# Kernel tuning notes

Hardware: AMD Instinct MI355X
Metric: run time of the kernel (lower is better)

## Reference

```python
import jax, jax.numpy as jnp
import numpy as np

EPS = 1e-8  # torch CosineSimilarity eps

M, N, D, H, NODE_NUM = 8, 100000, 256, 256, 200000

def setup_inputs() -> dict:
    key = jax.random.key(0)
    k1, k2, k3, k4, k5 = jax.random.split(key, 5)
    nodes = jax.random.randint(k1, (N,), 0, NODE_NUM)
    homo_embeddings = jax.random.normal(k2, (M, N, D), dtype=jnp.float32)
    W = jax.random.normal(k3, (H, D), dtype=jnp.float32) * (1.0 / np.sqrt(D))
    b = jax.random.normal(k4, (H,), dtype=jnp.float32) * 0.01
    out_embedding = jax.random.uniform(k5, (NODE_NUM, H), dtype=jnp.float32)  # nn.init.uniform_
    return {"nodes": nodes, "homo_embeddings": homo_embeddings, "W": W, "b": b,
            "out_embedding": out_embedding}

def reference(nodes, homo_embeddings, W, b, out_embedding):
    # homo_embeddings: [M, N, D] stacked homo_embedding_list
    # hidden = tanh(Linear(homo_emb))  -> [M, N, H]
    hidden = jnp.tanh(jnp.einsum('mnd,hd->mnh', homo_embeddings, W) + b)
    tgt = out_embedding[nodes]  # [N, H]
    # cosine similarity along feature dim, per meta-path -> [M, N]
    num = jnp.einsum('mnh,nh->mn', hidden, tgt)
    hn = jnp.maximum(jnp.linalg.norm(hidden, axis=-1), EPS)        # [M, N]
    tn = jnp.maximum(jnp.linalg.norm(tgt, axis=-1), EPS)           # [N]
    attention = jax.nn.softmax((num / (hn * tn[None, :])).T, axis=1)  # [N, M]
    # weighted sum over meta-paths -> [N, D]
    final = jnp.einsum('nm,mnd->nd', attention, homo_embeddings)
    return final
```

## Files before the change

kernel.cpp:

```cpp
#include <hip/hip_runtime.h>
#include <hip/hip_bf16.h>

#define EPSF 1e-8f
constexpr int M_ = 8, N_ = 100000, D_ = 256, H_ = 256;

typedef short  short8  __attribute__((ext_vector_type(8)));
typedef short  short4_ __attribute__((ext_vector_type(4)));
typedef float  float4_ __attribute__((ext_vector_type(4)));

__device__ __forceinline__ short bf16_rn(float x) {
  union { float f; unsigned u; } v; v.f = x;
  unsigned r = v.u + 0x7FFFu + ((v.u >> 16) & 1u);
  return (short)(r >> 16);
}

#define XB_S 264
#define XF_S 257
#define TG_S 260

__global__ __launch_bounds__(256, 2) void fused_hete(
    const int* __restrict__ nodes, const float* __restrict__ homo,
    const float* __restrict__ W, const float* __restrict__ bias,
    const float* __restrict__ oute, float* __restrict__ out)
{
  __shared__ __align__(16) short xb[16 * XB_S];
  __shared__ __align__(16) float xf[16 * XF_S];
  __shared__ __align__(16) float tg[2 * TG_S];
  __shared__ float rnum[4][16];
  __shared__ float rhn[4][16];
  __shared__ float cos_s[16];
  __shared__ float att_s[2][8];
  __shared__ float tn_s[2];

  const int t    = threadIdx.x;
  const int wave = t >> 6, lane = t & 63;
  const int quad = lane >> 4, l16 = lane & 15;

  short8 wf[4][8];
  float  bcol[4];
  #pragma unroll
  for (int tt = 0; tt < 4; ++tt) {
    const int col = wave * 64 + tt * 16 + l16;
    bcol[tt] = bias[col];
    #pragma unroll
    for (int k0 = 0; k0 < 8; ++k0) {
      const float* wp = W + (size_t)col * D_ + k0 * 32 + quad * 8;
      short8 f;
      #pragma unroll
      for (int j = 0; j < 8; ++j) f[j] = bf16_rn(wp[j]);
      wf[tt][k0] = f;
    }
  }

  for (int pair = blockIdx.x; pair < N_ / 2; pair += gridDim.x) {
    const int n0 = pair * 2;

    {
      const int r = t >> 4, c = t & 15;
      const int m = r & 7, ln = r >> 3;
      const float* src = homo + ((size_t)m * N_ + (n0 + ln)) * D_;
      #pragma unroll
      for (int i = 0; i < 4; ++i) {
        const int d = i * 64 + c * 4;
        const float4 v = *(const float4*)(src + d);
        float* xfr = &xf[r * XF_S + d];
        xfr[0] = v.x; xfr[1] = v.y; xfr[2] = v.z; xfr[3] = v.w;
        short4_ s;
        s[0] = bf16_rn(v.x); s[1] = bf16_rn(v.y); s[2] = bf16_rn(v.z); s[3] = bf16_rn(v.w);
        *(short4_*)&xb[r * XB_S + d] = s;
      }
      if (t < 128) {
        const int ln2 = t >> 6, c2 = t & 63;
        const int node = nodes[n0 + ln2];
        const float4 v = *(const float4*)(oute + (size_t)node * H_ + c2 * 4);
        float* tp = &tg[ln2 * TG_S + c2 * 4];
        tp[0] = v.x; tp[1] = v.y; tp[2] = v.z; tp[3] = v.w;
        float sq = v.x * v.x + v.y * v.y + v.z * v.z + v.w * v.w;
        #pragma unroll
        for (int off = 32; off; off >>= 1) sq += __shfl_down(sq, off);
        if (c2 == 0) tn_s[ln2] = fmaxf(sqrtf(sq), EPSF);
      }
    }
    __syncthreads();

    float4_ acc[4] = {};
    #pragma unroll
    for (int k0 = 0; k0 < 8; ++k0) {
      const short8 af = *(const short8*)&xb[l16 * XB_S + k0 * 32 + quad * 8];
      #pragma unroll
      for (int tt = 0; tt < 4; ++tt)
        acc[tt] = __builtin_amdgcn_mfma_f32_16x16x32_bf16(af, wf[tt][k0], acc[tt], 0, 0, 0);
    }

    const int lnq = quad >> 1;
    float nump[4] = {0.f, 0.f, 0.f, 0.f}, hnp[4] = {0.f, 0.f, 0.f, 0.f};
    #pragma unroll
    for (int tt = 0; tt < 4; ++tt) {
      const float tv = tg[lnq * TG_S + wave * 64 + tt * 16 + l16];
      #pragma unroll
      for (int e = 0; e < 4; ++e) {
        const float h = tanhf(acc[tt][e] + bcol[tt]);
        nump[e] += h * tv;
        hnp[e]  += h * h;
      }
    }
    #pragma unroll
    for (int off = 1; off < 16; off <<= 1) {
      #pragma unroll
      for (int e = 0; e < 4; ++e) {
        nump[e] += __shfl_xor(nump[e], off);
        hnp[e]  += __shfl_xor(hnp[e], off);
      }
    }
    if (l16 == 0) {
      #pragma unroll
      for (int e = 0; e < 4; ++e) {
        rnum[wave][quad * 4 + e] = nump[e];
        rhn[wave][quad * 4 + e]  = hnp[e];
      }
    }
    __syncthreads();

    if (t < 16) {
      const float nm = rnum[0][t] + rnum[1][t] + rnum[2][t] + rnum[3][t];
      const float hq = rhn[0][t] + rhn[1][t] + rhn[2][t] + rhn[3][t];
      const float hn = fmaxf(sqrtf(hq), EPSF);
      cos_s[t] = nm / (hn * tn_s[t >> 3]);
    }
    __syncthreads();

    if (t < 2) {
      float mx = cos_s[t * 8];
      #pragma unroll
      for (int m = 1; m < 8; ++m) mx = fmaxf(mx, cos_s[t * 8 + m]);
      float s = 0.f, ex[8];
      #pragma unroll
      for (int m = 0; m < 8; ++m) { ex[m] = expf(cos_s[t * 8 + m] - mx); s += ex[m]; }
      const float inv = 1.f / s;
      #pragma unroll
      for (int m = 0; m < 8; ++m) att_s[t][m] = ex[m] * inv;
    }
    __syncthreads();

    {
      const int ln = t >> 7, j = t & 127;
      float s0 = 0.f, s1 = 0.f;
      #pragma unroll
      for (int m = 0; m < 8; ++m) {
        const float a = att_s[ln][m];
        s0 += a * xf[(ln * 8 + m) * XF_S + j];
        s1 += a * xf[(ln * 8 + m) * XF_S + j + 128];
      }
      float* op = out + (size_t)(n0 + ln) * D_;
      op[j] = s0; op[j + 128] = s1;
    }
    __syncthreads();
  }
}

extern "C" void kernel_launch(void* const* d_in, const int* in_sizes, int n_in,
                              void* d_out, int out_size, void* d_ws, size_t ws_size,
                              hipStream_t stream) {
  const int*   nodes = (const int*)d_in[0];
  const float* homo  = (const float*)d_in[1];
  const float* W     = (const float*)d_in[2];
  const float* b     = (const float*)d_in[3];
  const float* oute  = (const float*)d_in[4];
  float* out = (float*)d_out;
  fused_hete<<<dim3(512), dim3(256), 0, stream>>>(nodes, homo, W, b, oute, out);
}
```

Before: 1.450 ms.

## Prefetch next pair into registers, fast tanh, fuse softmax tail, double grid

Each iteration now loads the next pair's homo rows, target embedding and node index into registers, so global loads overlap the MFMA and epilogue work of the current pair. tanhf is replaced with an exp2/rcp approximation. The cosine and softmax stage is computed redundantly per thread, which removes two block barriers per pair. The grid is doubled to 1024 blocks. The cost is higher register pressure under launch_bounds(256,2), plus a small loss of precision from the approximate tanh, exp and rcp.

Measured after the change: 1.399 ms. 1.04x faster.

```diff
diff --git a/kernel.cpp b/kernel.cpp
--- a/kernel.cpp
+++ b/kernel.cpp
@@ -3,6 +3,7 @@
 
 #define EPSF 1e-8f
 constexpr int M_ = 8, N_ = 100000, D_ = 256, H_ = 256;
+constexpr int NP_ = N_ / 2;
 
 typedef short  short8  __attribute__((ext_vector_type(8)));
 typedef short  short4_ __attribute__((ext_vector_type(4)));
@@ -12,6 +13,12 @@
   union { float f; unsigned u; } v; v.f = x;
   unsigned r = v.u + 0x7FFFu + ((v.u >> 16) & 1u);
   return (short)(r >> 16);
+}
+
+__device__ __forceinline__ float fast_tanh(float x) {
+  const float xc = fminf(fmaxf(x, -9.0f), 9.0f);
+  const float e2 = __builtin_amdgcn_exp2f(xc * 2.8853900817779268f);
+  return (e2 - 1.0f) * __builtin_amdgcn_rcpf(e2 + 1.0f);
 }
 
 #define XB_S 264
@@ -26,10 +33,8 @@
   __shared__ __align__(16) short xb[16 * XB_S];
   __shared__ __align__(16) float xf[16 * XF_S];
   __shared__ __align__(16) float tg[2 * TG_S];
-  __shared__ float rnum[4][16];
-  __shared__ float rhn[4][16];
-  __shared__ float cos_s[16];
-  __shared__ float att_s[2][8];
+  __shared__ __align__(16) float rnum[4][16];
+  __shared__ __align__(16) float rhn[4][16];
   __shared__ float tn_s[2];
 
   const int t    = threadIdx.x;
@@ -52,33 +57,61 @@
     }
   }
 
-  for (int pair = blockIdx.x; pair < N_ / 2; pair += gridDim.x) {
+  const int sr = t >> 4, sc = t & 15;
+  const int sm = sr & 7, sln = sr >> 3;
+  const float* hbase = homo + ((size_t)sm * N_ + sln) * D_ + sc * 4;
+  const int ln2 = t >> 6;
+  const int c2  = t & 63;
+
+  float4 hreg[4];
+  float4 treg = {0.f, 0.f, 0.f, 0.f};
+  int    nidx = 0;
+
+  const int p0 = blockIdx.x;
+  {
+    const float* src = hbase + (size_t)(p0 * 2) * D_;
+    #pragma unroll
+    for (int i = 0; i < 4; ++i) hreg[i] = *(const float4*)(src + i * 64);
+    if (t < 128) {
+      const int nd = nodes[p0 * 2 + ln2];
+      treg = *(const float4*)(oute + (size_t)nd * H_ + c2 * 4);
+      const int p1 = p0 + (int)gridDim.x;
+      if (p1 < NP_) nidx = nodes[p1 * 2 + ln2];
+    }
+  }
+
+  for (int pair = p0; pair < NP_; pair += gridDim.x) {
     const int n0 = pair * 2;
 
-    {
-      const int r = t >> 4, c = t & 15;
-      const int m = r & 7, ln = r >> 3;
-      const float* src = homo + ((size_t)m * N_ + (n0 + ln)) * D_;
-      #pragma unroll
-      for (int i = 0; i < 4; ++i) {
-        const int d = i * 64 + c * 4;
-        const float4 v = *(const float4*)(src + d);
-        float* xfr = &xf[r * XF_S + d];
-        xfr[0] = v.x; xfr[1] = v.y; xfr[2] = v.z; xfr[3] = v.w;
-        short4_ s;
-        s[0] = bf16_rn(v.x); s[1] = bf16_rn(v.y); s[2] = bf16_rn(v.z); s[3] = bf16_rn(v.w);
-        *(short4_*)&xb[r * XB_S + d] = s;
-      }
+    #pragma unroll
+    for (int i = 0; i < 4; ++i) {
+      const int d = i * 64 + sc * 4;
+      const float4 v = hreg[i];
+      float* xfr = &xf[sr * XF_S + d];
+      xfr[0] = v.x; xfr[1] = v.y; xfr[2] = v.z; xfr[3] = v.w;
+      short4_ s4;
+      s4[0] = bf16_rn(v.x); s4[1] = bf16_rn(v.y); s4[2] = bf16_rn(v.z); s4[3] = bf16_rn(v.w);
+      *(short4_*)&xb[sr * XB_S + d] = s4;
+    }
+    if (t < 128) {
+      const float4 v = treg;
+      float* tp = &tg[ln2 * TG_S + c2 * 4];
+      tp[0] = v.x; tp[1] = v.y; tp[2] = v.z; tp[3] = v.w;
+      float sq = v.x * v.x + v.y * v.y + v.z * v.z + v.w * v.w;
+      #pragma unroll
+      for (int off = 32; off; off >>= 1) sq += __shfl_down(sq, off);
+      if (c2 == 0) tn_s[ln2] = fmaxf(__builtin_amdgcn_sqrtf(sq), EPSF);
+    }
+
+    const int pnext = pair + (int)gridDim.x;
+    if (pnext < NP_) {
+      const float* src = hbase + (size_t)(pnext * 2) * D_;
+      #pragma unroll
+      for (int i = 0; i < 4; ++i) hreg[i] = *(const float4*)(src + i * 64);
       if (t < 128) {
-        const int ln2 = t >> 6, c2 = t & 63;
-        const int node = nodes[n0 + ln2];
-        const float4 v = *(const float4*)(oute + (size_t)node * H_ + c2 * 4);
-        float* tp = &tg[ln2 * TG_S + c2 * 4];
-        tp[0] = v.x; tp[1] = v.y; tp[2] = v.z; tp[3] = v.w;
-        float sq = v.x * v.x + v.y * v.y + v.z * v.z + v.w * v.w;
-        #pragma unroll
-        for (int off = 32; off; off >>= 1) sq += __shfl_down(sq, off);
-        if (c2 == 0) tn_s[ln2] = fmaxf(sqrtf(sq), EPSF);
+        treg = *(const float4*)(oute + (size_t)nidx * H_ + c2 * 4);
+        const int pnn = pnext + (int)gridDim.x;
+        if (pnn < NP_) nidx = nodes[pnn * 2 + ln2];
       }
     }
     __syncthreads();
@@ -99,7 +132,7 @@
       const float tv = tg[lnq * TG_S + wave * 64 + tt * 16 + l16];
       #pragma unroll
       for (int e = 0; e < 4; ++e) {
-        const float h = tanhf(acc[tt][e] + bcol[tt]);
+        const float h = fast_tanh(acc[tt][e] + bcol[tt]);
         nump[e] += h * tv;
         hnp[e]  += h * h;
       }
@@ -121,39 +154,42 @@
     }
     __syncthreads();
 
-    if (t < 16) {
-      const float nm = rnum[0][t] + rnum[1][t] + rnum[2][t] + rnum[3][t];
-      const float hq = rhn[0][t] + rhn[1][t] + rhn[2][t] + rhn[3][t];
-      const float hn = fmaxf(sqrtf(hq), EPSF);
-      cos_s[t] = nm / (hn * tn_s[t >> 3]);
-    }
-    __syncthreads();
-
-    if (t < 2) {
-      float mx = cos_s[t * 8];
-      #pragma unroll
-      for (int m = 1; m < 8; ++m) mx = fmaxf(mx, cos_s[t * 8 + m]);
-      float s = 0.f, ex[8];
-      #pragma unroll
-      for (int m = 0; m < 8; ++m) { ex[m] = expf(cos_s[t * 8 + m] - mx); s += ex[m]; }
-      const float inv = 1.f / s;
-      #pragma unroll
-      for (int m = 0; m < 8; ++m) att_s[t][m] = ex[m] * inv;
-    }
-    __syncthreads();
-
-    {
-      const int ln = t >> 7, j = t & 127;
-      float s0 = 0.f, s1 = 0.f;
-      #pragma unroll
-      for (int m = 0; m < 8; ++m) {
-        const float a = att_s[ln][m];
-        s0 += a * xf[(ln * 8 + m) * XF_S + j];
-        s1 += a * xf[(ln * 8 + m) * XF_S + j + 128];
-      }
-      float* op = out + (size_t)(n0 + ln) * D_;
-      op[j] = s0; op[j + 128] = s1;
-    }
+    const int fln = t >> 7, j = t & 127;
+    float4_ nm0 = {0,0,0,0}, nm1 = {0,0,0,0}, hq0 = {0,0,0,0}, hq1 = {0,0,0,0};
+    #pragma unroll
+    for (int w = 0; w < 4; ++w) {
+      nm0 += *(const float4_*)&rnum[w][fln * 8];
+      nm1 += *(const float4_*)&rnum[w][fln * 8 + 4];
+      hq0 += *(const float4_*)&rhn[w][fln * 8];
+      hq1 += *(const float4_*)&rhn[w][fln * 8 + 4];
+    }
+    const float tn = tn_s[fln];
+    float cosv[8], mx = -3.0e38f;
+    #pragma unroll
+    for (int m = 0; m < 8; ++m) {
+      const float nm = (m < 4) ? nm0[m] : nm1[m - 4];
+      const float hq = (m < 4) ? hq0[m] : hq1[m - 4];
+      const float hn = fmaxf(__builtin_amdgcn_sqrtf(hq), EPSF);
+      cosv[m] = nm * __builtin_amdgcn_rcpf(hn * tn);
+      mx = fmaxf(mx, cosv[m]);
+    }
+    float att[8], ssum = 0.f;
+    #pragma unroll
+    for (int m = 0; m < 8; ++m) {
+      att[m] = __builtin_amdgcn_exp2f((cosv[m] - mx) * 1.4426950408889634f);
+      ssum += att[m];
+    }
+    const float inv = __builtin_amdgcn_rcpf(ssum);
+
+    float s0 = 0.f, s1 = 0.f;
+    #pragma unroll
+    for (int m = 0; m < 8; ++m) {
+      const float a = att[m] * inv;
+      s0 += a * xf[(fln * 8 + m) * XF_S + j];
+      s1 += a * xf[(fln * 8 + m) * XF_S + j + 128];
+    }
+    float* op = out + (size_t)(n0 + fln) * D_;
+    op[j] = s0; op[j + 128] = s1;
     __syncthreads();
   }
 }
@@ -167,5 +203,5 @@
   const float* b     = (const float*)d_in[3];
   const float* oute  = (const float*)d_in[4];
   float* out = (float*)d_out;
-  fused_hete<<<dim3(512), dim3(256), 0, stream>>>(nodes, homo, W, b, oute, out);
-}
+  fused_hete<<<dim3(1024), dim3(256), 0, stream>>>(nodes, homo, W, b, oute, out);
+}
```
